# Kernel optimization log

Measured on AMD Instinct MI355X. Metric: run time of the kernel, lower is better.

## Reference

```python
import jax, jax.numpy as jnp
import numpy as np

B, H, S, D = 4, 16, 2048, 64

def setup_inputs() -> dict:
    key = jax.random.key(0)
    kq, kk, kv, km = jax.random.split(key, 4)
    Q = jax.random.normal(kq, (B, H, S, D), dtype=jnp.float32)
    K = jax.random.normal(kk, (B, H, S, D), dtype=jnp.float32)
    V = jax.random.normal(kv, (B, H, S, D), dtype=jnp.float32)
    mask = jax.random.randint(km, (B, 1, S, S), 0, 2, dtype=jnp.int32)
    return {"Q": Q, "K": K, "V": V, "mask": mask}

def reference(Q, K, V, mask):
    d_k = Q.shape[-1]
    scale = 1.0 / np.sqrt(d_k).astype(np.float32)
    # scores: [B, H, S, S]
    scores = jnp.einsum('bhqd,bhkd->bhqk', Q, K) * scale
    scores = jnp.where(mask == 0, -jnp.inf, scores)
    attn_weights = jax.nn.softmax(scores, axis=-1)
    # dropout rate 0.0 (eval) -> identity
    output = jnp.einsum('bhqk,bhkd->bhqd', attn_weights, V)
    return (output, attn_weights)
```

## Files before the change

### kernel.cpp

```cpp
#include <hip/hip_runtime.h>
#include <hip/hip_bf16.h>

#define SEQ   2048
#define DH    64
#define NBH   64
#define NH    16
#define QT    16
#define NW    8
#define NT    (NW * 64)
#define CHUNK 128
#define NCH   (SEQ / CHUNK)

typedef __attribute__((ext_vector_type(8))) short short8;
typedef __attribute__((ext_vector_type(4))) short short4v;
typedef __attribute__((ext_vector_type(4))) float f32x4;
typedef __attribute__((ext_vector_type(4))) int   i32x4;
typedef __attribute__((ext_vector_type(4))) unsigned short u16x4;

__device__ __forceinline__ unsigned short f2bf(float x) {
    union { float f; unsigned u; } c; c.f = x;
    return (unsigned short)((c.u + 0x7fffu + ((c.u >> 16) & 1u)) >> 16);
}
__device__ __forceinline__ unsigned pk2(float a, float b) {
    return (unsigned)f2bf(a) | ((unsigned)f2bf(b) << 16);
}
__device__ __forceinline__ float bf2f(short v) {
    return __uint_as_float((unsigned)(unsigned short)v << 16);
}

__device__ __forceinline__ void gl_lds16(const void* g, void* l) {
    __builtin_amdgcn_global_load_lds(
        (const __attribute__((address_space(1))) unsigned*)g,
        (__attribute__((address_space(3))) unsigned*)l, 16, 0, 0);
}

__global__ void prep_qk(const float* __restrict__ Q, const float* __restrict__ K,
                        unsigned short* __restrict__ Qb, unsigned short* __restrict__ Kb) {
    unsigned i4 = blockIdx.x * 256u + threadIdx.x;
    const float* src; unsigned short* dst;
    if (i4 < 2097152u) { src = Q; dst = Qb; }
    else { i4 -= 2097152u; src = K; dst = Kb; }
    f32x4 v = __builtin_nontemporal_load(&((const f32x4*)src)[i4]);
    u16x4 o; o[0] = f2bf(v[0]); o[1] = f2bf(v[1]); o[2] = f2bf(v[2]); o[3] = f2bf(v[3]);
    ((u16x4*)dst)[i4] = o;
}

__global__ void prep_v(const float* __restrict__ V, unsigned short* __restrict__ VT) {
    __shared__ unsigned short tile[64][72];
    const int t = threadIdx.x;
    const int bh = blockIdx.x >> 5;
    const int s0 = (blockIdx.x & 31) * 64;
    const float* vb = V + ((size_t)bh * SEQ + s0) * DH;
    #pragma unroll
    for (int pp = 0; pp < 4; ++pp) {
        const int sr = pp * 16 + (t >> 4);
        const int dc = (t & 15) * 4;
        f32x4 v = __builtin_nontemporal_load((const f32x4*)(vb + sr * DH + dc));
        tile[sr][dc]     = f2bf(v[0]); tile[sr][dc + 1] = f2bf(v[1]);
        tile[sr][dc + 2] = f2bf(v[2]); tile[sr][dc + 3] = f2bf(v[3]);
    }
    __syncthreads();
    const int d = t >> 2, c = (t & 3) * 16;
    short8 w0, w1;
    #pragma unroll
    for (int j = 0; j < 8; ++j) { w0[j] = (short)tile[c + j][d]; w1[j] = (short)tile[c + 8 + j][d]; }
    unsigned short* o = VT + ((size_t)bh * DH + d) * SEQ + s0 + c;
    *(short8*)o = w0; *(short8*)(o + 8) = w1;
}

__global__ void prep_m(const int* __restrict__ M, unsigned long long* __restrict__ M2) {
    __shared__ unsigned char mb[8][2048];
    const int t = threadIdx.x;
    const int row0 = blockIdx.x * 8;
    const i32x4* src = (const i32x4*)(M + (size_t)row0 * SEQ);
    #pragma unroll
    for (int i = 0; i < 16; ++i) {
        const int idx = i * 256 + t;
        i32x4 v = __builtin_nontemporal_load(&src[idx]);
        const int r = idx >> 9, c = (idx & 511) * 4;
        mb[r][c]     = (unsigned char)(v[0] != 0);
        mb[r][c + 1] = (unsigned char)(v[1] != 0);
        mb[r][c + 2] = (unsigned char)(v[2] != 0);
        mb[r][c + 3] = (unsigned char)(v[3] != 0);
    }
    __syncthreads();
    const int r = t >> 5, w = t & 31;
    const int wv = w >> 2, lg = w & 3;
    unsigned long long acc = 0ull;
    #pragma unroll
    for (int ci = 0; ci < 16; ++ci)
        #pragma unroll
        for (int rr = 0; rr < 4; ++rr)
            acc |= (unsigned long long)(mb[r][ci * 128 + 16 * wv + 4 * lg + rr] & 1)
                   << (4 * ci + rr);
    M2[(size_t)(row0 + r) * 32 + w] = acc;
}

__global__ __launch_bounds__(NT, 4) void attn_staged(
    const unsigned short* __restrict__ Qb, const unsigned short* __restrict__ Kb,
    const unsigned short* __restrict__ VT, const unsigned long long* __restrict__ M2,
    float* __restrict__ O, float* __restrict__ W)
{
    __shared__ union {
        short stage[2][16384];
        float part[NW][QT][68];
    } u;
    __shared__ float reds[NW * 16], rowRL[QT];

    const int tid = threadIdx.x, wv = tid >> 6, ln = tid & 63;
    const int lr = ln & 15, lg = ln >> 4;
    const int bid = blockIdx.x;
    const int h = bid & 15, t2 = bid >> 4;
    const int qt = t2 & 127, b = t2 >> 7;
    const int bh = b * NH + h, q0 = qt * QT;

    const float SC = 0.18033688011112042f;

    const unsigned short* qp = Qb + ((size_t)bh * SEQ + q0 + lr) * DH + 8 * lg;
    const short8 qf0 = *(const short8*)qp;
    const short8 qf1 = *(const short8*)(qp + 32);
    const unsigned long long mword = M2[((size_t)b * SEQ + q0 + lr) * 32 + wv * 4 + lg];

    const unsigned short* Kg = Kb + (size_t)bh * SEQ * DH;
    const unsigned short* Vg = VT + (size_t)bh * DH * SEQ;

    auto STAGE = [&](int ci, int bb) {
        const int cb = ci * CHUNK;
        #pragma unroll
        for (int jj = 0; jj < 2; ++jj) {
            const int j = 2 * wv + jj;
            const unsigned short* ks = Kg + (size_t)(cb + 8 * j + (ln >> 3)) * DH
                                          + (((ln & 7) ^ (ln >> 3)) << 3);
            gl_lds16(ks, (char*)&u.stage[bb][0] + j * 1024);
            const int d = 4 * j + (ln >> 4);
            const unsigned short* vs = Vg + (size_t)d * SEQ + cb
                                          + (((ln & 15) ^ (d & 7)) << 3);
            gl_lds16(vs, (char*)&u.stage[bb][8192] + j * 1024);
        }
    };

    STAGE(0, 0);
    __syncthreads();

    unsigned pe[2 * NCH];
    f32x4 acc[4] = {{0.f,0.f,0.f,0.f},{0.f,0.f,0.f,0.f},{0.f,0.f,0.f,0.f},{0.f,0.f,0.f,0.f}};
    float l = 0.f;

    #pragma unroll
    for (int ci = 0; ci < NCH; ++ci) {
        const int bb = ci & 1;
        if (ci + 1 < NCH) STAGE(ci + 1, bb ^ 1);

        const char* kb8 = (const char*)&u.stage[bb][0];
        const int krow = (16 * wv + lr) * 128;
        const short8 ka0 = *(const short8*)(kb8 + krow + (((lg)     ^ (lr & 7)) << 4));
        const short8 ka1 = *(const short8*)(kb8 + krow + (((4 + lg) ^ (lr & 7)) << 4));
        const char* vb8 = (const char*)&u.stage[bb][8192];
        const int vsl = ((4 * wv + lg) ^ (2 * (lr & 7))) << 3;
        short4v vv[4];
        #pragma unroll
        for (int nb = 0; nb < 4; ++nb)
            vv[nb] = *(const short4v*)(vb8 + (nb * 16 + lr) * 256 + vsl);

        f32x4 a = {0.f, 0.f, 0.f, 0.f};
        a = __builtin_amdgcn_mfma_f32_16x16x32_bf16(ka0, qf0, a, 0, 0, 0);
        a = __builtin_amdgcn_mfma_f32_16x16x32_bf16(ka1, qf1, a, 0, 0, 0);
        const unsigned nib = (unsigned)(mword >> (4 * ci)) & 0xFu;
        const float e0 = (nib & 1u) ? __builtin_amdgcn_exp2f(a[0] * SC) : 0.f;
        const float e1 = (nib & 2u) ? __builtin_amdgcn_exp2f(a[1] * SC) : 0.f;
        const float e2 = (nib & 4u) ? __builtin_amdgcn_exp2f(a[2] * SC) : 0.f;
        const float e3 = (nib & 8u) ? __builtin_amdgcn_exp2f(a[3] * SC) : 0.f;
        l += e0 + e1 + e2 + e3;
        pe[2 * ci]     = pk2(e0, e1);
        pe[2 * ci + 1] = pk2(e2, e3);
        union { uint2 w; short4v s; } pu;
        pu.w.x = pe[2 * ci]; pu.w.y = pe[2 * ci + 1];
        #pragma unroll
        for (int nb = 0; nb < 4; ++nb)
            acc[nb] = __builtin_amdgcn_mfma_f32_16x16x16bf16_1k(pu.s, vv[nb], acc[nb], 0, 0, 0);

        __syncthreads();
    }

    l += __shfl_xor(l, 16);
    l += __shfl_xor(l, 32);
    if (ln < 16) reds[wv * 16 + ln] = l;
    __syncthreads();

    float Lq = 0.f;
    #pragma unroll
    for (int w = 0; w < NW; ++w) Lq += reds[w * 16 + lr];
    const float rl = Lq > 0.f ? 1.f / Lq : 0.f;
    if (wv == 0 && ln < 16) rowRL[ln] = rl;

    {
        char* wb = (char*)&u.stage[0][0];
        const int rowbase = lr * 4096;
        const int sw = (lr & 7) << 5;
        #pragma unroll
        for (int ci = 0; ci < NCH; ++ci) {
            uint2 pk; pk.x = pe[2 * ci]; pk.y = pe[2 * ci + 1];
            const int cbyte = (ci * 256 + 32 * wv + 8 * lg) ^ sw;
            *(uint2*)(wb + rowbase + cbyte) = pk;
        }
    }
    __syncthreads();

    {
        const char* wb = (const char*)&u.stage[0][0];
        float* Wb = W + (size_t)bh * SEQ * SEQ + (size_t)q0 * SEQ;
        #pragma unroll
        for (int rr = 0; rr < 2; ++rr) {
            const int row = 2 * wv + rr;
            const char* rbase = wb + row * 4096;
            const int sw = (row & 7) << 5;
            const float wrl = rowRL[row];
            float* Wr = Wb + (size_t)row * SEQ;
            #pragma unroll
            for (int it = 0; it < 4; ++it) {
                short8 v = *(const short8*)(rbase + ((it * 1024 + ln * 16) ^ sw));
                f32x4 o0, o1;
                o0[0] = bf2f(v[0]) * wrl; o0[1] = bf2f(v[1]) * wrl;
                o0[2] = bf2f(v[2]) * wrl; o0[3] = bf2f(v[3]) * wrl;
                o1[0] = bf2f(v[4]) * wrl; o1[1] = bf2f(v[5]) * wrl;
                o1[2] = bf2f(v[6]) * wrl; o1[3] = bf2f(v[7]) * wrl;
                __builtin_nontemporal_store(o0, (f32x4*)(Wr + it * 512 + ln * 8));
                __builtin_nontemporal_store(o1, (f32x4*)(Wr + it * 512 + ln * 8 + 4));
            }
        }
    }
    __syncthreads();

    #pragma unroll
    for (int nb = 0; nb < 4; ++nb)
        #pragma unroll
        for (int r = 0; r < 4; ++r)
            u.part[wv][4 * lg + r][nb * 16 + lr] = acc[nb][r];
    __syncthreads();
    float* Ob = O + ((size_t)bh * SEQ + q0) * DH;
    for (int e = tid; e < QT * DH; e += NT) {
        const int q = e >> 6, d = e & 63;
        float s = 0.f;
        #pragma unroll
        for (int w = 0; w < NW; ++w) s += u.part[w][q][d];
        __builtin_nontemporal_store(s * rowRL[q], &Ob[e]);
    }
}

__global__ void attn_naive(const float* __restrict__ Q, const float* __restrict__ K,
                           const float* __restrict__ V, const int* __restrict__ M,
                           float* __restrict__ O, float* __restrict__ W) {
    __shared__ float sc[SEQ];
    __shared__ float red[256];
    const int bh = blockIdx.x >> 11, q = blockIdx.x & 2047, b = bh >> 4;
    const int t = threadIdx.x;
    const float* Qr = Q + ((size_t)bh * SEQ + q) * DH;
    const int* Mr = M + (size_t)b * SEQ * SEQ + (size_t)q * SEQ;
    for (int k = t; k < SEQ; k += 256) {
        const float* Kr = K + ((size_t)bh * SEQ + k) * DH;
        float s = 0.f;
        for (int d = 0; d < DH; ++d) s += Qr[d] * Kr[d];
        sc[k] = Mr[k] ? s * 0.125f : -INFINITY;
    }
    __syncthreads();
    float m = -INFINITY;
    for (int k = t; k < SEQ; k += 256) m = fmaxf(m, sc[k]);
    red[t] = m; __syncthreads();
    for (int o = 128; o; o >>= 1) { if (t < o) red[t] = fmaxf(red[t], red[t + o]); __syncthreads(); }
    m = red[0]; __syncthreads();
    float ls = 0.f;
    for (int k = t; k < SEQ; k += 256) { float e = __expf(sc[k] - m); sc[k] = e; ls += e; }
    red[t] = ls; __syncthreads();
    for (int o = 128; o; o >>= 1) { if (t < o) red[t] += red[t + o]; __syncthreads(); }
    const float rl = 1.f / red[0];
    float* Wr = W + (size_t)bh * SEQ * SEQ + (size_t)q * SEQ;
    for (int k = t; k < SEQ; k += 256) Wr[k] = sc[k] * rl;
    if (t < DH) {
        float o = 0.f;
        for (int k = 0; k < SEQ; ++k) o += sc[k] * V[((size_t)bh * SEQ + k) * DH + t];
        O[((size_t)bh * SEQ + q) * DH + t] = o * rl;
    }
}

extern "C" void kernel_launch(void* const* d_in, const int* in_sizes, int n_in,
                              void* d_out, int out_size, void* d_ws, size_t ws_size,
                              hipStream_t stream) {
    const float* Q = (const float*)d_in[0];
    const float* K = (const float*)d_in[1];
    const float* V = (const float*)d_in[2];
    const int*   M = (const int*)d_in[3];
    float* O = (float*)d_out;
    float* W = O + (size_t)NBH * SEQ * DH;

    const bool pre = ws_size >= (size_t)67108864;
    unsigned short* Qb = (unsigned short*)d_ws;
    unsigned short* Kb = Qb + (size_t)8388608;
    unsigned short* VT = Qb + (size_t)2 * 8388608;
    unsigned long long* M2 = (unsigned long long*)(Qb + (size_t)3 * 8388608);

    if (pre) {
        prep_qk<<<16384, 256, 0, stream>>>(Q, K, Qb, Kb);
        prep_v<<<2048, 256, 0, stream>>>(V, VT);
        prep_m<<<1024, 256, 0, stream>>>(M, M2);
        attn_staged<<<8192, NT, 0, stream>>>(Qb, Kb, VT, M2, O, W);
    } else {
        attn_naive<<<NBH * SEQ, 256, 0, stream>>>(Q, K, V, M, O, W);
    }
}
```

Baseline: 471.4 us.

## Precompute softmax row sums in a separate pass and stream normalized weights directly

Adds a rowsum kernel that computes QK^T exponentials once to get each row's normalizer, handling 128 query rows per block to reuse K tiles. The main attention kernel then normalizes each probability as it is produced and writes the weights straight to global memory inside the loop. This removes the LDS transpose/writeback epilogue and the in-kernel reduction. The cost is recomputing QK^T and exp for every score, plus weight stores that are only 16 bytes per lane instead of wide, coalesced rows.

```diff
diff --git a/kernel.cpp b/kernel.cpp
--- a/kernel.cpp
+++ b/kernel.cpp
@@ -24,9 +24,6 @@
 __device__ __forceinline__ unsigned pk2(float a, float b) {
     return (unsigned)f2bf(a) | ((unsigned)f2bf(b) << 16);
 }
-__device__ __forceinline__ float bf2f(short v) {
-    return __uint_as_float((unsigned)(unsigned short)v << 16);
-}
 
 __device__ __forceinline__ void gl_lds16(const void* g, void* l) {
     __builtin_amdgcn_global_load_lds(
@@ -96,16 +93,96 @@
     M2[(size_t)(row0 + r) * 32 + w] = acc;
 }
 
+__global__ __launch_bounds__(NT, 4) void rowsum(
+    const unsigned short* __restrict__ Qb, const unsigned short* __restrict__ Kb,
+    const unsigned long long* __restrict__ M2, float* __restrict__ RL)
+{
+    __shared__ short kst[2][8192];
+    __shared__ float reds[NW][16][8];
+
+    const int tid = threadIdx.x, wv = tid >> 6, ln = tid & 63;
+    const int lr = ln & 15, lg = ln >> 4;
+    const int bid = blockIdx.x;
+    const int h = bid & 15, qg = (bid >> 4) & 15, b = bid >> 8;
+    const int bh = b * NH + h, q0 = qg * 128;
+
+    const float SC = 0.18033688011112042f;
+
+    short8 qf[8][2];
+    unsigned long long mw[8];
+    #pragma unroll
+    for (int j = 0; j < 8; ++j) {
+        const unsigned short* qp = Qb + ((size_t)bh * SEQ + q0 + 16 * j + lr) * DH + 8 * lg;
+        qf[j][0] = *(const short8*)qp;
+        qf[j][1] = *(const short8*)(qp + 32);
+        mw[j] = M2[((size_t)b * SEQ + q0 + 16 * j + lr) * 32 + wv * 4 + lg];
+    }
+
+    const unsigned short* Kg = Kb + (size_t)bh * SEQ * DH;
+    auto STAGE = [&](int ci, int bb) {
+        const int cb = ci * CHUNK;
+        #pragma unroll
+        for (int jj = 0; jj < 2; ++jj) {
+            const int j = 2 * wv + jj;
+            const unsigned short* ks = Kg + (size_t)(cb + 8 * j + (ln >> 3)) * DH
+                                          + (((ln & 7) ^ (ln >> 3)) << 3);
+            gl_lds16(ks, (char*)&kst[bb][0] + j * 1024);
+        }
+    };
+
+    STAGE(0, 0);
+    __syncthreads();
+
+    float l[8] = {0.f, 0.f, 0.f, 0.f, 0.f, 0.f, 0.f, 0.f};
+    #pragma unroll
+    for (int ci = 0; ci < NCH; ++ci) {
+        const int bb = ci & 1;
+        if (ci + 1 < NCH) STAGE(ci + 1, bb ^ 1);
+        const char* kb8 = (const char*)&kst[bb][0];
+        const int krow = (16 * wv + lr) * 128;
+        const short8 ka0 = *(const short8*)(kb8 + krow + (((lg)     ^ (lr & 7)) << 4));
+        const short8 ka1 = *(const short8*)(kb8 + krow + (((4 + lg) ^ (lr & 7)) << 4));
+        #pragma unroll
+        for (int j = 0; j < 8; ++j) {
+            f32x4 a = {0.f, 0.f, 0.f, 0.f};
+            a = __builtin_amdgcn_mfma_f32_16x16x32_bf16(ka0, qf[j][0], a, 0, 0, 0);
+            a = __builtin_amdgcn_mfma_f32_16x16x32_bf16(ka1, qf[j][1], a, 0, 0, 0);
+            const unsigned nib = (unsigned)(mw[j] >> (4 * ci)) & 0xFu;
+            l[j] += ((nib & 1u) ? __builtin_amdgcn_exp2f(a[0] * SC) : 0.f)
+                  + ((nib & 2u) ? __builtin_amdgcn_exp2f(a[1] * SC) : 0.f)
+                  + ((nib & 4u) ? __builtin_amdgcn_exp2f(a[2] * SC) : 0.f)
+                  + ((nib & 8u) ? __builtin_amdgcn_exp2f(a[3] * SC) : 0.f);
+        }
+        __syncthreads();
+    }
+
+    #pragma unroll
+    for (int j = 0; j < 8; ++j) {
+        l[j] += __shfl_xor(l[j], 16);
+        l[j] += __shfl_xor(l[j], 32);
+    }
+    if (ln < 16) {
+        #pragma unroll
+        for (int j = 0; j < 8; ++j) reds[wv][ln][j] = l[j];
+    }
+    __syncthreads();
+    if (tid < 128) {
+        float s = 0.f;
+        #pragma unroll
+        for (int w = 0; w < NW; ++w) s += reds[w][tid & 15][tid >> 4];
+        RL[(size_t)bh * SEQ + q0 + tid] = s > 0.f ? 1.f / s : 0.f;
+    }
+}
+
 __global__ __launch_bounds__(NT, 4) void attn_staged(
     const unsigned short* __restrict__ Qb, const unsigned short* __restrict__ Kb,
     const unsigned short* __restrict__ VT, const unsigned long long* __restrict__ M2,
-    float* __restrict__ O, float* __restrict__ W)
+    const float* __restrict__ RL, float* __restrict__ O, float* __restrict__ W)
 {
     __shared__ union {
         short stage[2][16384];
         float part[NW][QT][68];
     } u;
-    __shared__ float reds[NW * 16], rowRL[QT];
 
     const int tid = threadIdx.x, wv = tid >> 6, ln = tid & 63;
     const int lr = ln & 15, lg = ln >> 4;
@@ -120,6 +197,7 @@
     const short8 qf0 = *(const short8*)qp;
     const short8 qf1 = *(const short8*)(qp + 32);
     const unsigned long long mword = M2[((size_t)b * SEQ + q0 + lr) * 32 + wv * 4 + lg];
+    const float rl = RL[(size_t)bh * SEQ + q0 + lr];
 
     const unsigned short* Kg = Kb + (size_t)bh * SEQ * DH;
     const unsigned short* Vg = VT + (size_t)bh * DH * SEQ;
@@ -142,9 +220,8 @@
     STAGE(0, 0);
     __syncthreads();
 
-    unsigned pe[2 * NCH];
     f32x4 acc[4] = {{0.f,0.f,0.f,0.f},{0.f,0.f,0.f,0.f},{0.f,0.f,0.f,0.f},{0.f,0.f,0.f,0.f}};
-    float l = 0.f;
+    float* Wp = W + (size_t)bh * SEQ * SEQ + (size_t)(q0 + lr) * SEQ + 16 * wv + 4 * lg;
 
     #pragma unroll
     for (int ci = 0; ci < NCH; ++ci) {
@@ -166,70 +243,20 @@
         a = __builtin_amdgcn_mfma_f32_16x16x32_bf16(ka0, qf0, a, 0, 0, 0);
         a = __builtin_amdgcn_mfma_f32_16x16x32_bf16(ka1, qf1, a, 0, 0, 0);
         const unsigned nib = (unsigned)(mword >> (4 * ci)) & 0xFu;
-        const float e0 = (nib & 1u) ? __builtin_amdgcn_exp2f(a[0] * SC) : 0.f;
-        const float e1 = (nib & 2u) ? __builtin_amdgcn_exp2f(a[1] * SC) : 0.f;
-        const float e2 = (nib & 4u) ? __builtin_amdgcn_exp2f(a[2] * SC) : 0.f;
-        const float e3 = (nib & 8u) ? __builtin_amdgcn_exp2f(a[3] * SC) : 0.f;
-        l += e0 + e1 + e2 + e3;
-        pe[2 * ci]     = pk2(e0, e1);
-        pe[2 * ci + 1] = pk2(e2, e3);
+        const float w0 = (nib & 1u) ? __builtin_amdgcn_exp2f(a[0] * SC) * rl : 0.f;
+        const float w1 = (nib & 2u) ? __builtin_amdgcn_exp2f(a[1] * SC) * rl : 0.f;
+        const float w2 = (nib & 4u) ? __builtin_amdgcn_exp2f(a[2] * SC) * rl : 0.f;
+        const float w3 = (nib & 8u) ? __builtin_amdgcn_exp2f(a[3] * SC) * rl : 0.f;
+        f32x4 wq; wq[0] = w0; wq[1] = w1; wq[2] = w2; wq[3] = w3;
+        __builtin_nontemporal_store(wq, (f32x4*)(Wp + ci * CHUNK));
         union { uint2 w; short4v s; } pu;
-        pu.w.x = pe[2 * ci]; pu.w.y = pe[2 * ci + 1];
+        pu.w.x = pk2(w0, w1); pu.w.y = pk2(w2, w3);
         #pragma unroll
         for (int nb = 0; nb < 4; ++nb)
             acc[nb] = __builtin_amdgcn_mfma_f32_16x16x16bf16_1k(pu.s, vv[nb], acc[nb], 0, 0, 0);
 
         __syncthreads();
     }
-
-    l += __shfl_xor(l, 16);
-    l += __shfl_xor(l, 32);
-    if (ln < 16) reds[wv * 16 + ln] = l;
-    __syncthreads();
-
-    float Lq = 0.f;
-    #pragma unroll
-    for (int w = 0; w < NW; ++w) Lq += reds[w * 16 + lr];
-    const float rl = Lq > 0.f ? 1.f / Lq : 0.f;
-    if (wv == 0 && ln < 16) rowRL[ln] = rl;
-
-    {
-        char* wb = (char*)&u.stage[0][0];
-        const int rowbase = lr * 4096;
-        const int sw = (lr & 7) << 5;
-        #pragma unroll
-        for (int ci = 0; ci < NCH; ++ci) {
-            uint2 pk; pk.x = pe[2 * ci]; pk.y = pe[2 * ci + 1];
-            const int cbyte = (ci * 256 + 32 * wv + 8 * lg) ^ sw;
-            *(uint2*)(wb + rowbase + cbyte) = pk;
-        }
-    }
-    __syncthreads();
-
-    {
-        const char* wb = (const char*)&u.stage[0][0];
-        float* Wb = W + (size_t)bh * SEQ * SEQ + (size_t)q0 * SEQ;
-        #pragma unroll
-        for (int rr = 0; rr < 2; ++rr) {
-            const int row = 2 * wv + rr;
-            const char* rbase = wb + row * 4096;
-            const int sw = (row & 7) << 5;
-            const float wrl = rowRL[row];
-            float* Wr = Wb + (size_t)row * SEQ;
-            #pragma unroll
-            for (int it = 0; it < 4; ++it) {
-                short8 v = *(const short8*)(rbase + ((it * 1024 + ln * 16) ^ sw));
-                f32x4 o0, o1;
-                o0[0] = bf2f(v[0]) * wrl; o0[1] = bf2f(v[1]) * wrl;
-                o0[2] = bf2f(v[2]) * wrl; o0[3] = bf2f(v[3]) * wrl;
-                o1[0] = bf2f(v[4]) * wrl; o1[1] = bf2f(v[5]) * wrl;
-                o1[2] = bf2f(v[6]) * wrl; o1[3] = bf2f(v[7]) * wrl;
-                __builtin_nontemporal_store(o0, (f32x4*)(Wr + it * 512 + ln * 8));
-                __builtin_nontemporal_store(o1, (f32x4*)(Wr + it * 512 + ln * 8 + 4));
-            }
-        }
-    }
-    __syncthreads();
 
     #pragma unroll
     for (int nb = 0; nb < 4; ++nb)
@@ -243,7 +270,7 @@
         float s = 0.f;
         #pragma unroll
         for (int w = 0; w < NW; ++w) s += u.part[w][q][d];
-        __builtin_nontemporal_store(s * rowRL[q], &Ob[e]);
+        __builtin_nontemporal_store(s, &Ob[e]);
     }
 }
 
@@ -297,12 +324,14 @@
     unsigned short* Kb = Qb + (size_t)8388608;
     unsigned short* VT = Qb + (size_t)2 * 8388608;
     unsigned long long* M2 = (unsigned long long*)(Qb + (size_t)3 * 8388608);
+    float* RL = (float*)((char*)d_ws + (size_t)52 * 1048576);
 
     if (pre) {
         prep_qk<<<16384, 256, 0, stream>>>(Q, K, Qb, Kb);
         prep_v<<<2048, 256, 0, stream>>>(V, VT);
         prep_m<<<1024, 256, 0, stream>>>(M, M2);
-        attn_staged<<<8192, NT, 0, stream>>>(Qb, Kb, VT, M2, O, W);
+        rowsum<<<1024, NT, 0, stream>>>(Qb, Kb, M2, RL);
+        attn_staged<<<8192, NT, 0, stream>>>(Qb, Kb, VT, M2, RL, O, W);
     } else {
         attn_naive<<<NBH * SEQ, 256, 0, stream>>>(Q, K, V, M, O, W);
     }
```

Measured after the change: 1.210 ms. 2.57x slower.

## Recompute attention weights in a second pass and single-buffer K/V staging

Applied to the files above, without the earlier changes.

Drops the per-thread register array of packed probabilities and the LDS transpose used to write the weights. After the row sums are known, a second pass recomputes QK^T from K read straight from global memory and writes normalized weights directly. K/V staging moves from double to single buffering, and the occupancy hint rises to 8 blocks. This frees LDS and registers for more resident blocks. The cost is redundant matmul and exp work, no load/compute overlap, and weight stores that form 64-byte row segments instead of full contiguous rows.

```diff
diff --git a/kernel.cpp b/kernel.cpp
--- a/kernel.cpp
+++ b/kernel.cpp
@@ -24,9 +24,6 @@
 __device__ __forceinline__ unsigned pk2(float a, float b) {
     return (unsigned)f2bf(a) | ((unsigned)f2bf(b) << 16);
 }
-__device__ __forceinline__ float bf2f(short v) {
-    return __uint_as_float((unsigned)(unsigned short)v << 16);
-}
 
 __device__ __forceinline__ void gl_lds16(const void* g, void* l) {
     __builtin_amdgcn_global_load_lds(
@@ -96,13 +93,13 @@
     M2[(size_t)(row0 + r) * 32 + w] = acc;
 }
 
-__global__ __launch_bounds__(NT, 4) void attn_staged(
+__global__ __launch_bounds__(NT, 8) void attn_staged(
     const unsigned short* __restrict__ Qb, const unsigned short* __restrict__ Kb,
     const unsigned short* __restrict__ VT, const unsigned long long* __restrict__ M2,
     float* __restrict__ O, float* __restrict__ W)
 {
     __shared__ union {
-        short stage[2][16384];
+        short stage[16384];
         float part[NW][QT][68];
     } u;
     __shared__ float reds[NW * 16], rowRL[QT];
@@ -124,38 +121,33 @@
     const unsigned short* Kg = Kb + (size_t)bh * SEQ * DH;
     const unsigned short* Vg = VT + (size_t)bh * DH * SEQ;
 
-    auto STAGE = [&](int ci, int bb) {
+    auto STAGE = [&](int ci) {
         const int cb = ci * CHUNK;
         #pragma unroll
         for (int jj = 0; jj < 2; ++jj) {
             const int j = 2 * wv + jj;
             const unsigned short* ks = Kg + (size_t)(cb + 8 * j + (ln >> 3)) * DH
                                           + (((ln & 7) ^ (ln >> 3)) << 3);
-            gl_lds16(ks, (char*)&u.stage[bb][0] + j * 1024);
+            gl_lds16(ks, (char*)&u.stage[0] + j * 1024);
             const int d = 4 * j + (ln >> 4);
             const unsigned short* vs = Vg + (size_t)d * SEQ + cb
                                           + (((ln & 15) ^ (d & 7)) << 3);
-            gl_lds16(vs, (char*)&u.stage[bb][8192] + j * 1024);
+            gl_lds16(vs, (char*)&u.stage[8192] + j * 1024);
         }
     };
 
-    STAGE(0, 0);
-    __syncthreads();
-
-    unsigned pe[2 * NCH];
     f32x4 acc[4] = {{0.f,0.f,0.f,0.f},{0.f,0.f,0.f,0.f},{0.f,0.f,0.f,0.f},{0.f,0.f,0.f,0.f}};
     float l = 0.f;
 
-    #pragma unroll
     for (int ci = 0; ci < NCH; ++ci) {
-        const int bb = ci & 1;
-        if (ci + 1 < NCH) STAGE(ci + 1, bb ^ 1);
-
-        const char* kb8 = (const char*)&u.stage[bb][0];
+        STAGE(ci);
+        __syncthreads();
+
+        const char* kb8 = (const char*)&u.stage[0];
         const int krow = (16 * wv + lr) * 128;
         const short8 ka0 = *(const short8*)(kb8 + krow + (((lg)     ^ (lr & 7)) << 4));
         const short8 ka1 = *(const short8*)(kb8 + krow + (((4 + lg) ^ (lr & 7)) << 4));
-        const char* vb8 = (const char*)&u.stage[bb][8192];
+        const char* vb8 = (const char*)&u.stage[8192];
         const int vsl = ((4 * wv + lg) ^ (2 * (lr & 7))) << 3;
         short4v vv[4];
         #pragma unroll
@@ -171,10 +163,8 @@
         const float e2 = (nib & 4u) ? __builtin_amdgcn_exp2f(a[2] * SC) : 0.f;
         const float e3 = (nib & 8u) ? __builtin_amdgcn_exp2f(a[3] * SC) : 0.f;
         l += e0 + e1 + e2 + e3;
-        pe[2 * ci]     = pk2(e0, e1);
-        pe[2 * ci + 1] = pk2(e2, e3);
         union { uint2 w; short4v s; } pu;
-        pu.w.x = pe[2 * ci]; pu.w.y = pe[2 * ci + 1];
+        pu.w.x = pk2(e0, e1); pu.w.y = pk2(e2, e3);
         #pragma unroll
         for (int nb = 0; nb < 4; ++nb)
             acc[nb] = __builtin_amdgcn_mfma_f32_16x16x16bf16_1k(pu.s, vv[nb], acc[nb], 0, 0, 0);
@@ -186,7 +176,6 @@
     l += __shfl_xor(l, 32);
     if (ln < 16) reds[wv * 16 + ln] = l;
     __syncthreads();
-
     float Lq = 0.f;
     #pragma unroll
     for (int w = 0; w < NW; ++w) Lq += reds[w * 16 + lr];
@@ -194,42 +183,24 @@
     if (wv == 0 && ln < 16) rowRL[ln] = rl;
 
     {
-        char* wb = (char*)&u.stage[0][0];
-        const int rowbase = lr * 4096;
-        const int sw = (lr & 7) << 5;
-        #pragma unroll
+        float* Wp = W + (size_t)bh * SEQ * SEQ + (size_t)(q0 + lr) * SEQ + 16 * wv + 4 * lg;
+        #pragma unroll 4
         for (int ci = 0; ci < NCH; ++ci) {
-            uint2 pk; pk.x = pe[2 * ci]; pk.y = pe[2 * ci + 1];
-            const int cbyte = (ci * 256 + 32 * wv + 8 * lg) ^ sw;
-            *(uint2*)(wb + rowbase + cbyte) = pk;
+            const unsigned short* kd = Kg + (size_t)(ci * CHUNK + 16 * wv + lr) * DH + 8 * lg;
+            const short8 ka0 = *(const short8*)kd;
+            const short8 ka1 = *(const short8*)(kd + 32);
+            f32x4 a = {0.f, 0.f, 0.f, 0.f};
+            a = __builtin_amdgcn_mfma_f32_16x16x32_bf16(ka0, qf0, a, 0, 0, 0);
+            a = __builtin_amdgcn_mfma_f32_16x16x32_bf16(ka1, qf1, a, 0, 0, 0);
+            const unsigned nib = (unsigned)(mword >> (4 * ci)) & 0xFu;
+            f32x4 wq;
+            wq[0] = (nib & 1u) ? __builtin_amdgcn_exp2f(a[0] * SC) * rl : 0.f;
+            wq[1] = (nib & 2u) ? __builtin_amdgcn_exp2f(a[1] * SC) * rl : 0.f;
+            wq[2] = (nib & 4u) ? __builtin_amdgcn_exp2f(a[2] * SC) * rl : 0.f;
+            wq[3] = (nib & 8u) ? __builtin_amdgcn_exp2f(a[3] * SC) * rl : 0.f;
+            __builtin_nontemporal_store(wq, (f32x4*)(Wp + ci * CHUNK));
         }
     }
-    __syncthreads();
-
-    {
-        const char* wb = (const char*)&u.stage[0][0];
-        float* Wb = W + (size_t)bh * SEQ * SEQ + (size_t)q0 * SEQ;
-        #pragma unroll
-        for (int rr = 0; rr < 2; ++rr) {
-            const int row = 2 * wv + rr;
-            const char* rbase = wb + row * 4096;
-            const int sw = (row & 7) << 5;
-            const float wrl = rowRL[row];
-            float* Wr = Wb + (size_t)row * SEQ;
-            #pragma unroll
-            for (int it = 0; it < 4; ++it) {
-                short8 v = *(const short8*)(rbase + ((it * 1024 + ln * 16) ^ sw));
-                f32x4 o0, o1;
-                o0[0] = bf2f(v[0]) * wrl; o0[1] = bf2f(v[1]) * wrl;
-                o0[2] = bf2f(v[2]) * wrl; o0[3] = bf2f(v[3]) * wrl;
-                o1[0] = bf2f(v[4]) * wrl; o1[1] = bf2f(v[5]) * wrl;
-                o1[2] = bf2f(v[6]) * wrl; o1[3] = bf2f(v[7]) * wrl;
-                __builtin_nontemporal_store(o0, (f32x4*)(Wr + it * 512 + ln * 8));
-                __builtin_nontemporal_store(o1, (f32x4*)(Wr + it * 512 + ln * 8 + 4));
-            }
-        }
-    }
-    __syncthreads();
 
     #pragma unroll
     for (int nb = 0; nb < 4; ++nb)
```

New measurement: 476.7 us. Within noise of the previous version (+1.1%).

## Give each wave private K/V staging and drop per-chunk block barriers

Applied to the files above, without the earlier changes.

Changes the V-transpose output layout to a chunk-blocked tiling, so each wave can load its own 16-key slice of K and V into a private double buffer. The per-chunk __syncthreads is replaced by explicit vmcnt/lgkmcnt waits, with prefetch two chunks ahead. The intent is to remove block-wide barrier stalls in the main loop and let waves run independently. The cost is reliance on hand-written waitcnt counts, which must exactly match the number of outstanding loads to stay correct.

```diff
diff --git a/kernel.cpp b/kernel.cpp
--- a/kernel.cpp
+++ b/kernel.cpp
@@ -64,7 +64,9 @@
     short8 w0, w1;
     #pragma unroll
     for (int j = 0; j < 8; ++j) { w0[j] = (short)tile[c + j][d]; w1[j] = (short)tile[c + 8 + j][d]; }
-    unsigned short* o = VT + ((size_t)bh * DH + d) * SEQ + s0 + c;
+    const int s = s0 + c;
+    unsigned short* o = VT + (size_t)bh * (SEQ * DH)
+                        + (size_t)(s >> 7) * 8192 + (size_t)((s >> 4) & 7) * 1024 + d * 16;
     *(short8*)o = w0; *(short8*)(o + 8) = w1;
 }
 
@@ -102,7 +104,8 @@
     float* __restrict__ O, float* __restrict__ W)
 {
     __shared__ union {
-        short stage[2][16384];
+        char  sbuf[NW][2][4096];
+        char  wmat[16][4096];
         float part[NW][QT][68];
     } u;
     __shared__ float reds[NW * 16], rowRL[QT];
@@ -120,27 +123,28 @@
     const short8 qf0 = *(const short8*)qp;
     const short8 qf1 = *(const short8*)(qp + 32);
     const unsigned long long mword = M2[((size_t)b * SEQ + q0 + lr) * 32 + wv * 4 + lg];
+    asm volatile("s_waitcnt vmcnt(0)" ::: "memory");
+    __builtin_amdgcn_sched_barrier(0);
 
     const unsigned short* Kg = Kb + (size_t)bh * SEQ * DH;
-    const unsigned short* Vg = VT + (size_t)bh * DH * SEQ;
+    const unsigned short* Vg = VT + (size_t)bh * (SEQ * DH);
 
     auto STAGE = [&](int ci, int bb) {
-        const int cb = ci * CHUNK;
-        #pragma unroll
-        for (int jj = 0; jj < 2; ++jj) {
-            const int j = 2 * wv + jj;
-            const unsigned short* ks = Kg + (size_t)(cb + 8 * j + (ln >> 3)) * DH
+        const int cb = ci * CHUNK + 16 * wv;
+        #pragma unroll
+        for (int tt = 0; tt < 2; ++tt) {
+            const unsigned short* ks = Kg + (size_t)(cb + 8 * tt + (ln >> 3)) * DH
                                           + (((ln & 7) ^ (ln >> 3)) << 3);
-            gl_lds16(ks, (char*)&u.stage[bb][0] + j * 1024);
-            const int d = 4 * j + (ln >> 4);
-            const unsigned short* vs = Vg + (size_t)d * SEQ + cb
-                                          + (((ln & 15) ^ (d & 7)) << 3);
-            gl_lds16(vs, (char*)&u.stage[bb][8192] + j * 1024);
+            gl_lds16(ks, &u.sbuf[wv][bb][tt * 1024]);
         }
+        const unsigned short* vsb = Vg + ci * 8192 + wv * 1024;
+        #pragma unroll
+        for (int hh = 0; hh < 2; ++hh)
+            gl_lds16(vsb + hh * 512 + ln * 8, &u.sbuf[wv][bb][2048 + hh * 1024]);
     };
 
     STAGE(0, 0);
-    __syncthreads();
+    STAGE(1, 1);
 
     unsigned pe[2 * NCH];
     f32x4 acc[4] = {{0.f,0.f,0.f,0.f},{0.f,0.f,0.f,0.f},{0.f,0.f,0.f,0.f},{0.f,0.f,0.f,0.f}};
@@ -149,18 +153,19 @@
     #pragma unroll
     for (int ci = 0; ci < NCH; ++ci) {
         const int bb = ci & 1;
-        if (ci + 1 < NCH) STAGE(ci + 1, bb ^ 1);
-
-        const char* kb8 = (const char*)&u.stage[bb][0];
-        const int krow = (16 * wv + lr) * 128;
-        const short8 ka0 = *(const short8*)(kb8 + krow + (((lg)     ^ (lr & 7)) << 4));
-        const short8 ka1 = *(const short8*)(kb8 + krow + (((4 + lg) ^ (lr & 7)) << 4));
-        const char* vb8 = (const char*)&u.stage[bb][8192];
-        const int vsl = ((4 * wv + lg) ^ (2 * (lr & 7))) << 3;
+        if (ci + 1 < NCH) asm volatile("s_waitcnt vmcnt(4)" ::: "memory");
+        else              asm volatile("s_waitcnt vmcnt(0)" ::: "memory");
+        __builtin_amdgcn_sched_barrier(0);
+
+        const char* kb8 = (const char*)&u.sbuf[wv][bb][0];
+        const int kro = (lr >> 3) * 1024 + (lr & 7) * 128;
+        const short8 ka0 = *(const short8*)(kb8 + kro + (((lg)     ^ (lr & 7)) << 4));
+        const short8 ka1 = *(const short8*)(kb8 + kro + (((4 + lg) ^ (lr & 7)) << 4));
+        const char* vb8 = (const char*)&u.sbuf[wv][bb][2048];
         short4v vv[4];
         #pragma unroll
         for (int nb = 0; nb < 4; ++nb)
-            vv[nb] = *(const short4v*)(vb8 + (nb * 16 + lr) * 256 + vsl);
+            vv[nb] = *(const short4v*)(vb8 + (nb * 16 + lr) * 32 + lg * 8);
 
         f32x4 a = {0.f, 0.f, 0.f, 0.f};
         a = __builtin_amdgcn_mfma_f32_16x16x32_bf16(ka0, qf0, a, 0, 0, 0);
@@ -179,7 +184,11 @@
         for (int nb = 0; nb < 4; ++nb)
             acc[nb] = __builtin_amdgcn_mfma_f32_16x16x16bf16_1k(pu.s, vv[nb], acc[nb], 0, 0, 0);
 
-        __syncthreads();
+        if (ci + 2 < NCH) {
+            asm volatile("s_waitcnt lgkmcnt(0)" ::: "memory");
+            __builtin_amdgcn_sched_barrier(0);
+            STAGE(ci + 2, bb);
+        }
     }
 
     l += __shfl_xor(l, 16);
@@ -194,7 +203,7 @@
     if (wv == 0 && ln < 16) rowRL[ln] = rl;
 
     {
-        char* wb = (char*)&u.stage[0][0];
+        char* wb = &u.wmat[0][0];
         const int rowbase = lr * 4096;
         const int sw = (lr & 7) << 5;
         #pragma unroll
@@ -207,7 +216,7 @@
     __syncthreads();
 
     {
-        const char* wb = (const char*)&u.stage[0][0];
+        const char* wb = &u.wmat[0][0];
         float* Wb = W + (size_t)bh * SEQ * SEQ + (size_t)q0 * SEQ;
         #pragma unroll
         for (int rr = 0; rr < 2; ++rr) {
```

Measured after the change: 413.1 us. 12.4% less time.
